# Performance work log

Measured on AMD Instinct MI355X. Metric: run time of the kernel, lower is better.

The kernel has to match this reference:

```python
import jax, jax.numpy as jnp
import numpy as np

# Cell hyperparameters (from model.cell / Eprop_fit.__init__)
THRESHOLD = 0.6
DAMPENING = 0.3
N_REF = 5
DECAY = 0.8          # membrane decay used for pre-synaptic trace filters
ELIG_DECAY = 0.8     # default decay in exp_convolve for eligibility filtering
REG = 300.0


def exp_convolve(t, decay):
    """Causal exponential filter along time axis 1: a_t = decay*a_{t-1} + x_t."""
    xt = jnp.moveaxis(t, 1, 0)  # time-major [T, B, ...]

    def step(acc, cur):
        acc = acc * decay + cur
        return acc, acc

    _, y = jax.lax.scan(step, jnp.zeros_like(xt[0]), xt)
    return jnp.moveaxis(y, 0, 1)


def refractory_count(z, n_ref):
    """ref_count[t] depends on z[:t]; starts at 0."""
    zt = jnp.moveaxis(jax.lax.stop_gradient(z), 1, 0)  # [T, B, N]
    init = jnp.zeros(zt.shape[1:], jnp.int32)

    def step(c, zc):
        c = jnp.where(zc > 0, jnp.int32(n_ref - 1), jnp.maximum(0, c - 1))
        return c, c

    _, counts = jax.lax.scan(step, init, zt[:-1])
    counts = jnp.concatenate([init[None], counts], axis=0)
    return jnp.moveaxis(counts, 0, 1)  # [B, T, N]


def setup_inputs() -> dict:
    key = jax.random.key(0)
    k1, k2, k3, k4, k5, k6 = jax.random.split(key, 6)
    B, T, N, NIN, K = 4, 300, 200, 100, 10
    v = jax.random.normal(k1, (B, T, N), jnp.float32) * 0.5 + 0.3
    z = (jax.random.uniform(k2, (B, T, N)) < 0.05).astype(jnp.float32)  # spikes
    x = (jax.random.uniform(k3, (B, T, NIN)) < 0.1).astype(jnp.float32)
    error1 = jax.random.normal(k4, (B, T, K), jnp.float32) * 0.1   # output error
    error2 = jax.random.normal(k5, (N,), jnp.float32) * 0.01       # firing-rate error
    w_out = jax.random.normal(k6, (N, K), jnp.float32) / np.sqrt(N)
    return {"v": v, "z": z, "x": x, "error1": error1, "error2": error2, "w_out": w_out}


def reference(v, z, x, error1, error2, w_out):
    B, T, N = v.shape

    v_scaled = (v - THRESHOLD) / THRESHOLD
    psi_no_ref = DAMPENING * jnp.maximum(1.0 - jnp.abs(v_scaled), 0.0) / THRESHOLD

    ref = refractory_count(z, N_REF)
    post_term = jnp.where(ref > 0, 0.0, psi_no_ref)  # [B, T, N]

    # shift z by one time step (z_{t-1}, zero-initialized)
    z_prev = jnp.concatenate([jnp.zeros_like(z[:, :1]), z[:, :-1]], axis=1)

    pre_w_in = exp_convolve(x, DECAY)        # x_bar  [B, T, n_in]
    pre_w_rec = exp_convolve(z_prev, DECAY)  # z_bar  [B, T, N]
    pre_w_out = exp_convolve(z, DECAY)       # [B, T, N]

    # eligibility traces: [B, T, pre, post]
    et_in = post_term[:, :, None, :] * pre_w_in[:, :, :, None]
    et_rec = post_term[:, :, None, :] * pre_w_rec[:, :, :, None]

    fet_in = exp_convolve(et_in, ELIG_DECAY)
    fet_rec = exp_convolve(et_rec, ELIG_DECAY)

    avg_in = jnp.mean(et_in, axis=(0, 1))    # [n_in, N]
    avg_rec = jnp.mean(et_rec, axis=(0, 1))  # [N, N]

    # learning signals (symmetric e-prop): L = error @ w_out^T
    learning_signals = jnp.einsum('btk,jk->btj', error1, w_out)  # [B, T, N]

    dloss_dw_out = jnp.einsum('btk,btj->jk', error1, pre_w_out)          # [N, K]
    dloss_dw_in = jnp.einsum('btj,btij->ij', learning_signals, fet_in)   # [n_in, N]
    dloss_dw_rec = jnp.einsum('btj,btij->ij', learning_signals, fet_rec) # [N, N]

    dloss_dw_in = dloss_dw_in + REG * (error2 * avg_in)
    dloss_dw_rec = dloss_dw_rec + REG * (error2 * avg_rec)

    # mask autapses (diagonal of recurrent weight gradient)
    eye = jnp.eye(N, dtype=bool)
    dloss_dw_rec = jnp.where(eye, 0.0, dloss_dw_rec)

    return dloss_dw_in, dloss_dw_rec, dloss_dw_out
```

## Files before the change

kernel.cpp:

```cpp
#include <hip/hip_runtime.h>

#define BB    4
#define TT    300
#define NN    200
#define NINN  100
#define KK    10
#define DECAY 0.8f
#define THR   0.6f
#define DAMP  0.3f

#define LCH   20
#define NCHK  (TT / LCH)
#define WARM  48

#define SK    24
#define KCH   (BB * TT / SK)

#define XBAR_OFF  0
#define ZFILT_OFF (BB*TT*NINN)
#define ZBAR_OFF  (ZFILT_OFF + BB*TT*NN)
#define CBUF_OFF  (ZBAR_OFF  + BB*TT*NN)
#define GBAR_OFF  (CBUF_OFF  + BB*TT*NN)

#define R_A_BASE  0
#define R_A_N     (BB*NCHK*NINN)
#define R_B_BASE  6144
#define R_B_N     (BB*NCHK*NN)
#define R_G_BASE  18176
#define R_G_N     (BB*NCHK*KK)
#define R_Z_BASE  18944
#define R_Z_N     15500
#define K1_TOTAL  (R_Z_BASE + R_Z_N)

__global__ void scan_kernel(const float* __restrict__ z,
                            const float* __restrict__ x,
                            const float* __restrict__ error1,
                            float* __restrict__ ws,
                            float* __restrict__ out) {
    int tid = blockIdx.x * blockDim.x + threadIdx.x;
    float* xbar  = ws + XBAR_OFF;
    float* zfilt = ws + ZFILT_OFF;
    float* zbar  = ws + ZBAR_OFF;
    float* gbar  = ws + GBAR_OFF;

    if (tid < R_A_N) {
        int i = tid % NINN, r = tid / NINN;
        int chunk = r % NCHK, b = r / NCHK;
        int t0 = chunk * LCH;
        const float* src = x + (size_t)b * TT * NINN + i;
        float acc = 0.f;
        #pragma unroll
        for (int d = WARM; d >= 1; --d) {
            int t = t0 - d;
            int tc = t < 0 ? 0 : t;
            float val = src[tc * NINN];
            acc = DECAY * acc + (t < 0 ? 0.f : val);
        }
        float vals[LCH];
        #pragma unroll
        for (int tt = 0; tt < LCH; ++tt) vals[tt] = src[(t0 + tt) * NINN];
        #pragma unroll
        for (int tt = 0; tt < LCH; ++tt) { acc = DECAY * acc + vals[tt]; vals[tt] = acc; }
        float* dst = xbar + (size_t)b * TT * NINN + i;
        #pragma unroll
        for (int tt = 0; tt < LCH; ++tt) dst[(t0 + tt) * NINN] = vals[tt];
    } else if (tid >= R_B_BASE && tid < R_B_BASE + R_B_N) {
        int u = tid - R_B_BASE;
        int j = u % NN, r = u / NN;
        int chunk = r % NCHK, b = r / NCHK;
        int t0 = chunk * LCH;
        const float* src = z + (size_t)b * TT * NN + j;
        float acc = 0.f;
        #pragma unroll
        for (int d = WARM; d >= 1; --d) {
            int t = t0 - d;
            int tc = t < 0 ? 0 : t;
            float val = src[tc * NN];
            acc = DECAY * acc + (t < 0 ? 0.f : val);
        }
        float zv[LCH], pre[LCH];
        #pragma unroll
        for (int tt = 0; tt < LCH; ++tt) zv[tt] = src[(t0 + tt) * NN];
        #pragma unroll
        for (int tt = 0; tt < LCH; ++tt) {
            pre[tt] = acc;
            acc = DECAY * acc + zv[tt];
            zv[tt] = acc;
        }
        float* dzb = zbar  + (size_t)b * TT * NN + j;
        float* dzf = zfilt + (size_t)b * TT * NN + j;
        #pragma unroll
        for (int tt = 0; tt < LCH; ++tt) dzb[(t0 + tt) * NN] = pre[tt];
        #pragma unroll
        for (int tt = 0; tt < LCH; ++tt) dzf[(t0 + tt) * NN] = zv[tt];
    } else if (tid >= R_G_BASE && tid < R_G_BASE + R_G_N) {
        int u = tid - R_G_BASE;
        int k = u % KK, r = u / KK;
        int chunk = r % NCHK, b = r / NCHK;
        int t0 = chunk * LCH, t1 = t0 + LCH - 1;
        const float* src = error1 + (size_t)b * TT * KK + k;
        float G = 0.f;
        #pragma unroll
        for (int d = WARM; d >= 1; --d) {
            int t = t1 + d;
            int tc = t > TT - 1 ? TT - 1 : t;
            float val = src[tc * KK];
            G = DECAY * G + (t > TT - 1 ? 0.f : val);
        }
        float ev[LCH];
        #pragma unroll
        for (int tt = 0; tt < LCH; ++tt) ev[tt] = src[(t1 - tt) * KK];
        float* dst = gbar + (size_t)b * TT * KK + k;
        #pragma unroll
        for (int tt = 0; tt < LCH; ++tt) {
            G = DECAY * G + ev[tt];
            dst[(t1 - tt) * KK] = G;
        }
    } else if (tid >= R_Z_BASE && tid < R_Z_BASE + R_Z_N) {
        int u = tid - R_Z_BASE;
        ((float4*)out)[u] = make_float4(0.f, 0.f, 0.f, 0.f);
    }
}

__global__ void c_kernel(const float* __restrict__ v,
                         const float* __restrict__ z,
                         const float* __restrict__ error2,
                         const float* __restrict__ w_out,
                         float* __restrict__ ws) {
    int tid = blockIdx.x * blockDim.x + threadIdx.x;
    if (tid >= BB * TT * NN) return;
    const float* gbar = ws + GBAR_OFF;
    float* cbuf = ws + CBUF_OFF;

    int j = tid % NN, bt = tid / NN;
    int t = bt % TT, b = bt / TT;

    float Ldot = 0.f;
    #pragma unroll
    for (int k = 0; k < KK; ++k)
        Ldot += gbar[bt * KK + k] * w_out[j * KK + k];
    float coeff = 0.25f * error2[j];

    bool refr = false;
    #pragma unroll
    for (int d = 1; d <= 4; ++d) {
        int s = t - d;
        int sc = s < 0 ? 0 : s;
        float zv = z[(b * TT + sc) * NN + j];
        if (s >= 0 && zv > 0.f) refr = true;
    }
    float vv = v[bt * NN + j];
    float vs = (vv - THR) / THR;
    float psi = (DAMP / THR) * fmaxf(1.f - fabsf(vs), 0.f);
    cbuf[bt * NN + j] = (refr ? 0.f : psi) * (Ldot + coeff);
}

#define R3_MAIN_N  (SK * 75 * 50)
#define R3_TAIL_BASE 90112
#define R3_TAIL_N  (SK * NN * KK)

__global__ void out_kernel(const float* __restrict__ error1,
                           const float* __restrict__ ws,
                           float* __restrict__ out) {
    int tid = blockIdx.x * blockDim.x + threadIdx.x;
    const float* xbar  = ws + XBAR_OFF;
    const float* zfilt = ws + ZFILT_OFF;
    const float* zbar  = ws + ZBAR_OFF;
    const float* cbuf  = ws + CBUF_OFF;

    if (tid < R3_MAIN_N) {
        int jq = tid % 50, r = tid / 50;
        int pg = r % 75, s = r / 75;
        int j0 = jq * 4, p0 = pg * 4;
        int btBase = s * KCH;

        bool isrec = (p0 >= NINN);
        const float* A = isrec ? (zbar + (p0 - NINN)) : (xbar + p0);
        int lda = isrec ? NN : NINN;

        float4 acc0 = make_float4(0,0,0,0), acc1 = acc0, acc2 = acc0, acc3 = acc0;
        #pragma unroll 10
        for (int rr = 0; rr < KCH; ++rr) {
            int bt = btBase + rr;
            float4 av = *(const float4*)(A + (size_t)bt * lda);
            float4 cv = *(const float4*)(cbuf + (size_t)bt * NN + j0);
            acc0.x += av.x * cv.x; acc0.y += av.x * cv.y; acc0.z += av.x * cv.z; acc0.w += av.x * cv.w;
            acc1.x += av.y * cv.x; acc1.y += av.y * cv.y; acc1.z += av.y * cv.z; acc1.w += av.y * cv.w;
            acc2.x += av.z * cv.x; acc2.y += av.z * cv.y; acc2.z += av.z * cv.z; acc2.w += av.z * cv.w;
            acc3.x += av.w * cv.x; acc3.y += av.w * cv.y; acc3.z += av.w * cv.z; acc3.w += av.w * cv.w;
        }
        float accs[4][4] = {
            {acc0.x, acc0.y, acc0.z, acc0.w},
            {acc1.x, acc1.y, acc1.z, acc1.w},
            {acc2.x, acc2.y, acc2.z, acc2.w},
            {acc3.x, acc3.y, acc3.z, acc3.w}};
        if (!isrec) {
            float* o = out + (size_t)p0 * NN + j0;
            #pragma unroll
            for (int a = 0; a < 4; ++a)
                #pragma unroll
                for (int bb = 0; bb < 4; ++bb)
                    atomicAdd(o + a * NN + bb, accs[a][bb]);
        } else {
            int i0 = p0 - NINN;
            float* o = out + NINN * NN + (size_t)i0 * NN + j0;
            #pragma unroll
            for (int a = 0; a < 4; ++a)
                #pragma unroll
                for (int bb = 0; bb < 4; ++bb)
                    if (i0 + a != j0 + bb)
                        atomicAdd(o + a * NN + bb, accs[a][bb]);
        }
    } else if (tid >= R3_TAIL_BASE && tid < R3_TAIL_BASE + R3_TAIL_N) {
        int u = tid - R3_TAIL_BASE;
        int k = u % KK, r = u / KK;
        int j = r % NN, s = r / NN;
        int btBase = s * KCH;
        float acc = 0.f;
        #pragma unroll 10
        for (int rr = 0; rr < KCH; ++rr) {
            int bt = btBase + rr;
            acc += zfilt[bt * NN + j] * error1[bt * KK + k];
        }
        atomicAdd(out + NINN * NN + NN * NN + j * KK + k, acc);
    }
}

extern "C" void kernel_launch(void* const* d_in, const int* in_sizes, int n_in,
                              void* d_out, int out_size, void* d_ws, size_t ws_size,
                              hipStream_t stream) {
    const float* v  = (const float*)d_in[0];
    const float* z  = (const float*)d_in[1];
    const float* x  = (const float*)d_in[2];
    const float* e1 = (const float*)d_in[3];
    const float* e2 = (const float*)d_in[4];
    const float* wo = (const float*)d_in[5];
    float* out = (float*)d_out;
    float* ws  = (float*)d_ws;

    scan_kernel<<<(K1_TOTAL + 255) / 256, 256, 0, stream>>>(z, x, e1, ws, out);

    c_kernel<<<(BB * TT * NN + 255) / 256, 256, 0, stream>>>(v, z, e2, wo, ws);

    int n3 = R3_TAIL_BASE + R3_TAIL_N;
    out_kernel<<<(n3 + 255) / 256, 256, 0, stream>>>(e1, ws, out);
}
```

Baseline: 105.0 us.

## Replace atomic split-K output GEMM with in-block shared-memory reduction

The output kernel now assigns each block a 4-row by 64-column tile of the weight gradients. Its 16 split-K slices are reduced through shared memory and written directly with plain stores, which removes the float atomics and most of the zeroing of the output buffer. The w_out gradient tail uses 6 splits of 200 timesteps instead of 24, so it issues fewer atomics. The trade-off is less parallelism in the main GEMM (300 blocks), plus some idle threads in the last column tile.

```diff
diff --git a/kernel.cpp b/kernel.cpp
--- a/kernel.cpp
+++ b/kernel.cpp
@@ -13,23 +13,19 @@
 #define NCHK  (TT / LCH)
 #define WARM  48
 
-#define SK    24
-#define KCH   (BB * TT / SK)
-
 #define XBAR_OFF  0
 #define ZFILT_OFF (BB*TT*NINN)
 #define ZBAR_OFF  (ZFILT_OFF + BB*TT*NN)
 #define CBUF_OFF  (ZBAR_OFF  + BB*TT*NN)
 #define GBAR_OFF  (CBUF_OFF  + BB*TT*NN)
 
-#define R_A_BASE  0
 #define R_A_N     (BB*NCHK*NINN)
 #define R_B_BASE  6144
 #define R_B_N     (BB*NCHK*NN)
 #define R_G_BASE  18176
 #define R_G_N     (BB*NCHK*KK)
 #define R_Z_BASE  18944
-#define R_Z_N     15500
+#define R_Z_N     500
 #define K1_TOTAL  (R_Z_BASE + R_Z_N)
 
 __global__ void scan_kernel(const float* __restrict__ z,
@@ -118,7 +114,7 @@
         }
     } else if (tid >= R_Z_BASE && tid < R_Z_BASE + R_Z_N) {
         int u = tid - R_Z_BASE;
-        ((float4*)out)[u] = make_float4(0.f, 0.f, 0.f, 0.f);
+        ((float4*)(out + NINN * NN + NN * NN))[u] = make_float4(0.f, 0.f, 0.f, 0.f);
     }
 }
 
@@ -155,74 +151,93 @@
     cbuf[bt * NN + j] = (refr ? 0.f : psi) * (Ldot + coeff);
 }
 
-#define R3_MAIN_N  (SK * 75 * 50)
-#define R3_TAIL_BASE 90112
-#define R3_TAIL_N  (SK * NN * KK)
+#define SKB 16
+#define KC3 (BB * TT / SKB)
+#define PT  4
+#define JT  64
 
 __global__ void out_kernel(const float* __restrict__ error1,
                            const float* __restrict__ ws,
                            float* __restrict__ out) {
-    int tid = blockIdx.x * blockDim.x + threadIdx.x;
+    __shared__ float red[SKB * PT * JT];
+    int bid = blockIdx.x;
+    int tid = threadIdx.x;
     const float* xbar  = ws + XBAR_OFF;
     const float* zfilt = ws + ZFILT_OFF;
     const float* zbar  = ws + ZBAR_OFF;
     const float* cbuf  = ws + CBUF_OFF;
 
-    if (tid < R3_MAIN_N) {
-        int jq = tid % 50, r = tid / 50;
-        int pg = r % 75, s = r / 75;
-        int j0 = jq * 4, p0 = pg * 4;
-        int btBase = s * KCH;
-
-        bool isrec = (p0 >= NINN);
-        const float* A = isrec ? (zbar + (p0 - NINN)) : (xbar + p0);
-        int lda = isrec ? NN : NINN;
-
-        float4 acc0 = make_float4(0,0,0,0), acc1 = acc0, acc2 = acc0, acc3 = acc0;
-        #pragma unroll 10
-        for (int rr = 0; rr < KCH; ++rr) {
-            int bt = btBase + rr;
-            float4 av = *(const float4*)(A + (size_t)bt * lda);
-            float4 cv = *(const float4*)(cbuf + (size_t)bt * NN + j0);
-            acc0.x += av.x * cv.x; acc0.y += av.x * cv.y; acc0.z += av.x * cv.z; acc0.w += av.x * cv.w;
-            acc1.x += av.y * cv.x; acc1.y += av.y * cv.y; acc1.z += av.y * cv.z; acc1.w += av.y * cv.w;
-            acc2.x += av.z * cv.x; acc2.y += av.z * cv.y; acc2.z += av.z * cv.z; acc2.w += av.z * cv.w;
-            acc3.x += av.w * cv.x; acc3.y += av.w * cv.y; acc3.z += av.w * cv.z; acc3.w += av.w * cv.w;
-        }
-        float accs[4][4] = {
-            {acc0.x, acc0.y, acc0.z, acc0.w},
-            {acc1.x, acc1.y, acc1.z, acc1.w},
-            {acc2.x, acc2.y, acc2.z, acc2.w},
-            {acc3.x, acc3.y, acc3.z, acc3.w}};
-        if (!isrec) {
-            float* o = out + (size_t)p0 * NN + j0;
+    if (bid < 300) {
+        int pt = bid >> 2;
+        int jt = bid & 3;
+        int p0 = pt * PT;
+        int j0 = jt * JT;
+        int W = NN - j0; if (W > JT) W = JT;
+        int jq = tid & 15;
+        int s  = tid >> 4;
+
+        if (jq * 4 < W) {
+            bool isrec = (p0 >= NINN);
+            const float* A = isrec ? (zbar + (p0 - NINN)) : (xbar + p0);
+            int lda = isrec ? NN : NINN;
+            const float* C = cbuf + j0 + jq * 4;
+            int bt0 = s * KC3;
+            float acc[4][4];
             #pragma unroll
             for (int a = 0; a < 4; ++a)
                 #pragma unroll
-                for (int bb = 0; bb < 4; ++bb)
-                    atomicAdd(o + a * NN + bb, accs[a][bb]);
-        } else {
-            int i0 = p0 - NINN;
-            float* o = out + NINN * NN + (size_t)i0 * NN + j0;
+                for (int c = 0; c < 4; ++c) acc[a][c] = 0.f;
+            #pragma unroll 5
+            for (int rr = 0; rr < KC3; ++rr) {
+                int bt = bt0 + rr;
+                float4 av = *(const float4*)(A + (size_t)bt * lda);
+                float4 cv = *(const float4*)(C + (size_t)bt * NN);
+                float am[4] = {av.x, av.y, av.z, av.w};
+                float cm[4] = {cv.x, cv.y, cv.z, cv.w};
+                #pragma unroll
+                for (int a = 0; a < 4; ++a)
+                    #pragma unroll
+                    for (int c = 0; c < 4; ++c) acc[a][c] += am[a] * cm[c];
+            }
+            float* dst = red + s * (PT * JT) + jq * 4;
             #pragma unroll
             for (int a = 0; a < 4; ++a)
-                #pragma unroll
-                for (int bb = 0; bb < 4; ++bb)
-                    if (i0 + a != j0 + bb)
-                        atomicAdd(o + a * NN + bb, accs[a][bb]);
-        }
-    } else if (tid >= R3_TAIL_BASE && tid < R3_TAIL_BASE + R3_TAIL_N) {
-        int u = tid - R3_TAIL_BASE;
-        int k = u % KK, r = u / KK;
-        int j = r % NN, s = r / NN;
-        int btBase = s * KCH;
-        float acc = 0.f;
-        #pragma unroll 10
-        for (int rr = 0; rr < KCH; ++rr) {
-            int bt = btBase + rr;
-            acc += zfilt[bt * NN + j] * error1[bt * KK + k];
-        }
-        atomicAdd(out + NINN * NN + NN * NN + j * KK + k, acc);
+                *(float4*)(dst + a * JT) =
+                    make_float4(acc[a][0], acc[a][1], acc[a][2], acc[a][3]);
+        }
+        __syncthreads();
+
+        int o = tid;
+        int pl = o >> 6, jl = o & 63;
+        if (jl < W) {
+            float sum = 0.f;
+            #pragma unroll
+            for (int s2 = 0; s2 < SKB; ++s2) sum += red[s2 * (PT * JT) + o];
+            int row = p0 + pl;
+            int j = j0 + jl;
+            if (row < NINN) {
+                out[row * NN + j] = sum;
+            } else {
+                int i = row - NINN;
+                out[NINN * NN + i * NN + j] = (i == j) ? 0.f : sum;
+            }
+        }
+    } else {
+        int u = (bid - 300) * 256 + tid;
+        if (u < 6 * NN * KK) {
+            int jk = u % (NN * KK);
+            int s = u / (NN * KK);
+            int j = jk % NN;
+            int k = jk / NN;
+            int bt0 = s * 200;
+            float acc = 0.f;
+            #pragma unroll 8
+            for (int rr = 0; rr < 200; ++rr) {
+                int bt = bt0 + rr;
+                acc += zfilt[bt * NN + j] * error1[bt * KK + k];
+            }
+            atomicAdd(out + NINN * NN + NN * NN + j * KK + k, acc);
+        }
     }
 }
 
@@ -242,6 +257,5 @@
 
     c_kernel<<<(BB * TT * NN + 255) / 256, 256, 0, stream>>>(v, z, e2, wo, ws);
 
-    int n3 = R3_TAIL_BASE + R3_TAIL_N;
-    out_kernel<<<(n3 + 255) / 256, 256, 0, stream>>>(e1, ws, out);
-}
+    out_kernel<<<347, 256, 0, stream>>>(e1, ws, out);
+}
```

Result: faster. 87.48 us (-16.7%).
